# Kernel optimization log

Hardware: AMD Instinct MI355X
Metric: run time of the kernel (lower is better)

Reference implementation:

```python
import jax, jax.numpy as jnp
import numpy as np

B, S, H, D = 4, 1024, 16, 64
DIM = H * D          # 1024
FF_INNER = 4 * DIM   # 4096
ROT_BASE = 1000.0


def _l2norm(x):
    # F.normalize(p=2, dim=-1): x / max(||x||_2, 1e-12)
    n = jnp.linalg.norm(x, axis=-1, keepdims=True)
    return x / jnp.maximum(n, 1e-12)


def _rmsnorm(x):
    return x * jax.lax.rsqrt(jnp.mean(x * x, axis=-1, keepdims=True) + jnp.finfo(jnp.float32).eps)


def _rope_tables(seq, d, base):
    inv_freq = base ** (-(jnp.arange(0, d, 2, dtype=jnp.float32) / d))
    freqs = jnp.outer(jnp.arange(seq, dtype=jnp.float32), inv_freq)  # [S, D/2]
    # original caches cos/sin in bfloat16
    cos = jnp.cos(freqs).astype(jnp.bfloat16)[None, :, None, :]
    sin = jnp.sin(freqs).astype(jnp.bfloat16)[None, :, None, :]
    return cos, sin


def _rope(x, cos, sin):
    d = x.shape[3] // 2
    x1, x2 = x[..., :d], x[..., d:]
    y1 = x1 * cos + x2 * sin
    y2 = -x1 * sin + x2 * cos
    return jnp.concatenate([y1, y2], axis=3).astype(x.dtype)


def setup_inputs() -> dict:
    key = jax.random.key(0)
    ks = jax.random.split(key, 12)
    w = lambda k, shp: 0.02 * jax.random.normal(k, shp, dtype=jnp.float32)
    inp = {
        'h_states': jax.random.normal(ks[0], (B, S, DIM), dtype=jnp.float32),
        'attention_mask': jnp.tril(jnp.ones((S, S), dtype=jnp.float32))[None].repeat(B, axis=0),
        'Wq': w(ks[1], (DIM, DIM)), 'Wk': w(ks[2], (DIM, DIM)), 'Wv': w(ks[3], (DIM, DIM)),
        'WqB': w(ks[4], (DIM, DIM)), 'WkB': w(ks[5], (DIM, DIM)),
        'Wo': w(ks[6], (DIM, DIM)), 'bo': jnp.zeros((DIM,), jnp.float32),
        'Wff_in': w(ks[7], (DIM, 2 * FF_INNER)), 'bff_in': jnp.zeros((2 * FF_INNER,), jnp.float32),
        'Wff_out': w(ks[8], (FF_INNER, DIM)), 'bff_out': jnp.zeros((DIM,), jnp.float32),
        'learnedlambda': jnp.asarray(1.0, jnp.float32),
        'l2normscale': jnp.log(jnp.asarray(float(S) ** 2 - float(S), jnp.float32)),
    }
    return inp


def reference(h_states, attention_mask, Wq, Wk, Wv, WqB, WkB, Wo, bo,
              Wff_in, bff_in, Wff_out, bff_out, learnedlambda, l2normscale):
    inner = _rmsnorm(h_states)                               # layerwisenorm (rmsnorm, no affine)
    scale = D ** -0.5

    def proj(Wm):
        return (inner @ Wm).reshape(B, S, H, D)
    q, k, v = proj(Wq), proj(Wk), proj(Wv)
    bq, bk = proj(WqB), proj(WkB)

    cos, sin = _rope_tables(S, D, ROT_BASE)
    q = _rope(_l2norm(q), cos, sin)
    k = _rope(_l2norm(k), cos, sin)
    bq = _rope(_l2norm(bq), cos, sin)
    bk = _rope(_l2norm(bk), cos, sin)

    # main branch: causal softmax attention, scale=1, scaled by learned l2normscale
    scores = jnp.einsum('bihd,bjhd->bhij', q, k)             # [B,H,S,S]
    causal = jnp.tril(jnp.ones((S, S), dtype=bool))
    scores = jnp.where(causal, scores, -jnp.inf)
    attn = jax.nn.softmax(scores, axis=-1)
    y = l2normscale * jnp.einsum('bhij,bjhd->bihd', attn, v)  # [B,S,H,D]

    # bias branch: softmax-free masked scores @ ones == row-sum broadcast over D
    bscores = jnp.einsum('bihd,bjhd->bhij', bq, bk) * scale
    bscores = bscores * attention_mask[:, None, :, :]
    brow = bscores.sum(axis=-1)                               # [B,H,S]
    y = y + jnp.transpose(brow, (0, 2, 1))[..., None]         # broadcast over D

    attn_out = y.reshape(B, S, DIM) @ Wo + bo

    # SwiGLU FFN: chunk -> x, gate; silu(gate) * x
    u = inner @ Wff_in + bff_in
    xh, gate = jnp.split(u, 2, axis=-1)
    dense_out = (jax.nn.silu(gate) * xh) @ Wff_out + bff_out

    return h_states * learnedlambda + dense_out + attn_out
```

## Files before the change

### kernel.cpp

```cpp
#include <hip/hip_runtime.h>
#include <stdint.h>
#include <math.h>

typedef float f32x4 __attribute__((ext_vector_type(4)));
typedef short s16x8 __attribute__((ext_vector_type(8)));
typedef unsigned short bfu;

#define AS1q const __attribute__((address_space(1))) void*
#define AS3q __attribute__((address_space(3))) void*

static __device__ __forceinline__ float bf2f(bfu v) {
  return __uint_as_float(((unsigned int)v) << 16);
}
static __device__ __forceinline__ bfu f2bf(float f) {
  unsigned int u = __float_as_uint(f);
  return (bfu)((u + 0x7fffu + ((u >> 16) & 1u)) >> 16);
}

template <int MODE>
__global__ __launch_bounds__(256) void wconv_t(const float* __restrict__ W, bfu* __restrict__ Wt,
                                               int K, int N, int dstride, int dofs) {
  __shared__ float t[32][33];
  int tx = threadIdx.x & 31, ty = threadIdx.x >> 5;
  int nb = blockIdx.x * 32, kb = blockIdx.y * 32;
#pragma unroll
  for (int i = 0; i < 4; i++) {
    int r = ty + i * 8;
    t[r][tx] = W[(size_t)(kb + r) * N + nb + tx];
  }
  __syncthreads();
#pragma unroll
  for (int i = 0; i < 4; i++) {
    int r = ty + i * 8;
    int n = nb + r;
    int nd;
    if (MODE == 1) {
      int j = n & 4095, isg = n >> 12;
      nd = ((j >> 4) << 5) | (isg << 4) | (j & 15);
    } else nd = n;
    int k = kb + tx;
    int kp = (MODE == 2) ? (((k >> 5) << 5) | ((k & 15) << 1) | ((k >> 4) & 1)) : k;
    Wt[(size_t)nd * dstride + dofs + kp] = f2bf(t[tx][r]);
  }
}

struct Ptr5 { const float* p[5]; };
__global__ __launch_bounds__(256) void wconv5(Ptr5 srcs, bfu* __restrict__ dst) {
  __shared__ float t[32][33];
  const float* W = srcs.p[blockIdx.z];
  bfu* Wt = dst + ((size_t)blockIdx.z << 20);
  int tx = threadIdx.x & 31, ty = threadIdx.x >> 5;
  int nb = blockIdx.x * 32, kb = blockIdx.y * 32;
#pragma unroll
  for (int i = 0; i < 4; i++) {
    int r = ty + i * 8;
    t[r][tx] = W[(size_t)(kb + r) * 1024 + nb + tx];
  }
  __syncthreads();
#pragma unroll
  for (int i = 0; i < 4; i++) {
    int r = ty + i * 8;
    Wt[(size_t)(nb + r) * 1024 + kb + tx] = f2bf(t[tx][r]);
  }
}

__global__ void rope_tab(bfu* __restrict__ ct, bfu* __restrict__ st) {
  int idx = blockIdx.x * 256 + threadIdx.x;
  int s = idx >> 5, i = idx & 31;
  float f = powf(1000.0f, -(float)i / 32.0f);
  float fr = (float)s * f;
  ct[idx] = f2bf(cosf(fr));
  st[idx] = f2bf(sinf(fr));
}

__global__ __launch_bounds__(256) void rmsnorm_k(const float* __restrict__ h, bfu* __restrict__ inner) {
  int row = blockIdx.x;
  const float* hr = h + (size_t)row * 1024;
  f32x4 x = *reinterpret_cast<const f32x4*>(hr + threadIdx.x * 4);
  float ss = x[0] * x[0] + x[1] * x[1] + x[2] * x[2] + x[3] * x[3];
  for (int off = 32; off; off >>= 1) ss += __shfl_down(ss, off);
  __shared__ float wsum[4];
  int wave = threadIdx.x >> 6, lane = threadIdx.x & 63;
  if (lane == 0) wsum[wave] = ss;
  __syncthreads();
  float tot = wsum[0] + wsum[1] + wsum[2] + wsum[3];
  float r = rsqrtf(tot * (1.0f / 1024.0f) + 1.1920929e-07f);
  bfu* o = inner + (size_t)row * 1024 + threadIdx.x * 4;
  o[0] = f2bf(x[0] * r); o[1] = f2bf(x[1] * r);
  o[2] = f2bf(x[2] * r); o[3] = f2bf(x[3] * r);
}

template <int EPI>
__global__ __launch_bounds__(512, 2) void gemm256p(const bfu* __restrict__ A, const bfu* __restrict__ Bt,
                                                   bfu* __restrict__ outB,
                                                   const float* __restrict__ bias,
                                                   int M, int N, int K, int rbm, int rbn) {
  __shared__ __align__(16) char lds[131072];
  int nbx = N >> 8;
  int c = blockIdx.x & 7, rr = blockIdx.x >> 3;
  int ca = nbx / rbn;
  int bn0 = (c % ca) * rbn, bm0 = (c / ca) * rbm;
  int bm = bm0 + rr / rbn, bn = bn0 + rr % rbn;
  int tid = threadIdx.x, w = tid >> 6, lane = tid & 63;
  int wm = w >> 2, wn = w & 3;
  int g = lane >> 4, l15 = lane & 15;
  int NT = K >> 6;
  int NI = NT >> 1;

  f32x4 acc[8][4];
#pragma unroll
  for (int m = 0; m < 8; m++)
#pragma unroll
    for (int n = 0; n < 4; n++) acc[m][n] = (f32x4){0.f, 0.f, 0.f, 0.f};

  s16x8 af[4][2];
  s16x8 bfr[4][2];

  auto stage = [&](int mat, int kt, int hf) {
    if (kt >= NT) return;
    int d = kt & 1;
    const bfu* s0 = (mat == 0) ? A : Bt;
    int rowbase = ((mat == 0) ? bm : bn) * 256 + hf * 128;
    int k0 = kt << 6;
    char* base = lds + d * 65536 + mat * 32768 + hf * 16384;
#pragma unroll
    for (int r = 0; r < 2; r++) {
      int L = r * 512 + tid;
      int row = L >> 3, cc = L & 7;
      int kc = cc ^ (row & 7);
      const bfu* src = s0 + (size_t)(rowbase + row) * K + k0 + kc * 8;
      char* dst = base + r * 8192 + w * 1024;
      __builtin_amdgcn_global_load_lds((AS1q)src, (AS3q)dst, 16, 0, 0);
    }
  };

  auto ldA = [&](int d, int mh) {
    const char* base = lds + d * 65536 + wm * 16384;
#pragma unroll
    for (int mm = 0; mm < 4; mm++) {
      int row = mh * 64 + mm * 16 + l15;
#pragma unroll
      for (int ks = 0; ks < 2; ks++)
        af[mm][ks] = *reinterpret_cast<const s16x8*>(
            base + row * 128 + (((ks * 4 + g) ^ (row & 7)) << 4));
    }
  };
  auto ldB2 = [&](int d, int nh) {
    const char* base = lds + d * 65536 + 32768 + (wn >> 1) * 16384;
#pragma unroll
    for (int nn = 0; nn < 2; nn++) {
      int row = (wn & 1) * 64 + (nh * 2 + nn) * 16 + l15;
#pragma unroll
      for (int ks = 0; ks < 2; ks++)
        bfr[nh * 2 + nn][ks] = *reinterpret_cast<const s16x8*>(
            base + row * 128 + (((ks * 4 + g) ^ (row & 7)) << 4));
    }
  };
  auto mfma_q = [&](int mh, int nh) {
    asm volatile("s_waitcnt lgkmcnt(0)" ::: "memory");
    __builtin_amdgcn_sched_barrier(0);
    __builtin_amdgcn_s_barrier();
    __builtin_amdgcn_s_setprio(1);
#pragma unroll
    for (int mm = 0; mm < 4; mm++)
#pragma unroll
      for (int nn = 0; nn < 2; nn++) {
        int n = nh * 2 + nn, m = mh * 4 + mm;
#pragma unroll
        for (int ks = 0; ks < 2; ks++)
          acc[m][n] = __builtin_amdgcn_mfma_f32_16x16x32_bf16(af[mm][ks], bfr[n][ks], acc[m][n], 0, 0, 0);
      }
    __builtin_amdgcn_s_setprio(0);
    __builtin_amdgcn_sched_barrier(0);
  };

  stage(1, 0, 0); stage(0, 0, 0); stage(0, 0, 1); stage(1, 0, 1);
  stage(1, 1, 0); stage(1, 1, 1);
  asm volatile("s_waitcnt vmcnt(4)" ::: "memory");
  __builtin_amdgcn_s_barrier();
  __builtin_amdgcn_sched_barrier(0);

  for (int i = 0; i < NI; i++) {
    int t0 = 2 * i, t1 = 2 * i + 1;
    ldA(0, 0); ldB2(0, 0);
    stage(0, t1, 0);
    mfma_q(0, 0);
    ldB2(0, 1);
    stage(0, t1, 1);
    mfma_q(0, 1);
    ldA(0, 1);
    stage(1, t0 + 2, 0);
    mfma_q(1, 0);
    stage(1, t0 + 2, 1);
    mfma_q(1, 1);
    asm volatile("s_waitcnt vmcnt(4)" ::: "memory");
    __builtin_amdgcn_s_barrier();
    __builtin_amdgcn_sched_barrier(0);
    ldA(1, 0); ldB2(1, 0);
    stage(0, t0 + 2, 0);
    mfma_q(0, 0);
    ldB2(1, 1);
    stage(0, t0 + 2, 1);
    mfma_q(0, 1);
    ldA(1, 1);
    stage(1, t1 + 2, 0);
    mfma_q(1, 0);
    stage(1, t1 + 2, 1);
    mfma_q(1, 1);
    asm volatile("s_waitcnt vmcnt(4)" ::: "memory");
    __builtin_amdgcn_s_barrier();
    __builtin_amdgcn_sched_barrier(0);
  }

  int j0 = (bn * 8 + wn * 2) * 16 + l15;
  float bx0 = bias[j0], bg0 = bias[j0 + 4096];
  float bx1 = bias[j0 + 16], bg1 = bias[j0 + 16 + 4096];
  int cb = (bn * 4 + wn) * 32 + 2 * l15;
#pragma unroll
  for (int m = 0; m < 8; m++) {
#pragma unroll
    for (int r = 0; r < 4; r++) {
      int row = bm * 256 + wm * 128 + m * 16 + g * 4 + r;
      float xh0 = acc[m][0][r] + bx0, gt0 = acc[m][1][r] + bg0;
      float xh1 = acc[m][2][r] + bx1, gt1 = acc[m][3][r] + bg1;
      float s0 = gt0 / (1.0f + __expf(-gt0)) * xh0;
      float s1 = gt1 / (1.0f + __expf(-gt1)) * xh1;
      unsigned int pk = (unsigned int)f2bf(s0) | ((unsigned int)f2bf(s1) << 16);
      *reinterpret_cast<unsigned int*>(outB + (size_t)row * 5120 + cb) = pk;
    }
  }
}

__global__ __launch_bounds__(256, 3) void gemm128p(const bfu* __restrict__ A, const bfu* __restrict__ Bt,
                                                   bfu* __restrict__ qb, bfu* __restrict__ kb,
                                                   bfu* __restrict__ vb,
                                                   bfu* __restrict__ bqh, bfu* __restrict__ bkh,
                                                   const bfu* __restrict__ ct, const bfu* __restrict__ st,
                                                   int M, int N, int K, int rbm, int rbn) {
  __shared__ __align__(16) char lds[49152];
  int nbx = N >> 7;
  int c = blockIdx.x & 7, rr = blockIdx.x >> 3;
  int ca = nbx / rbn;
  int bn0 = (c % ca) * rbn, bm0 = (c / ca) * rbm;
  int bm = bm0 + rr / rbn, bn = bn0 + rr % rbn;
  int tid = threadIdx.x, w = tid >> 6, lane = tid & 63;
  int wm = w >> 1, wn = w & 1;
  int g = lane >> 4, l15 = lane & 15;
  int NT = K >> 5;

  f32x4 acc[4][4];
#pragma unroll
  for (int m = 0; m < 4; m++)
#pragma unroll
    for (int n = 0; n < 4; n++) acc[m][n] = (f32x4){0.f, 0.f, 0.f, 0.f};

  auto stage = [&](int buf, int t) {
    int k0 = t << 5;
#pragma unroll
    for (int r = 0; r < 2; r++) {
      int L = r * 256 + tid;
      int row = L >> 2, cc = L & 3;
      int kc = cc ^ (row & 3);
      const bfu* srcA = A + (size_t)(bm * 128 + row) * K + k0 + kc * 8;
      char* dstA = lds + buf * 16384 + r * 4096 + w * 1024;
      __builtin_amdgcn_global_load_lds((AS1q)srcA, (AS3q)dstA, 16, 0, 0);
      const bfu* srcB = Bt + (size_t)(bn * 128 + row) * K + k0 + kc * 8;
      char* dstB = lds + buf * 16384 + 8192 + r * 4096 + w * 1024;
      __builtin_amdgcn_global_load_lds((AS1q)srcB, (AS3q)dstB, 16, 0, 0);
    }
  };

  stage(0, 0); stage(1, 1);
  asm volatile("s_waitcnt vmcnt(4)" ::: "memory");
  __builtin_amdgcn_s_barrier();
  __builtin_amdgcn_sched_barrier(0);

  int bc = 0;
  for (int t = 0; t < NT; t++) {
    int bs = bc + 2; if (bs >= 3) bs -= 3;
    if (t + 2 < NT) stage(bs, t + 2);
    const char* la = lds + bc * 16384;
    const char* lb = la + 8192;
    s16x8 af[4], bfr[4];
#pragma unroll
    for (int m = 0; m < 4; m++) {
      int row = wm * 64 + m * 16 + l15;
      af[m] = *reinterpret_cast<const s16x8*>(la + row * 64 + ((g ^ (row & 3)) << 4));
    }
#pragma unroll
    for (int n = 0; n < 4; n++) {
      int row = wn * 64 + n * 16 + l15;
      bfr[n] = *reinterpret_cast<const s16x8*>(lb + row * 64 + ((g ^ (row & 3)) << 4));
    }
    asm volatile("s_waitcnt lgkmcnt(0)" ::: "memory");
    __builtin_amdgcn_sched_barrier(0);
    __builtin_amdgcn_s_setprio(1);
#pragma unroll
    for (int m = 0; m < 4; m++)
#pragma unroll
      for (int n = 0; n < 4; n++)
        acc[m][n] = __builtin_amdgcn_mfma_f32_16x16x32_bf16(af[m], bfr[n], acc[m][n], 0, 0, 0);
    __builtin_amdgcn_s_setprio(0);
    __builtin_amdgcn_sched_barrier(0);
    if (t < NT - 2) { asm volatile("s_waitcnt vmcnt(4)" ::: "memory"); }
    else            { asm volatile("s_waitcnt vmcnt(0)" ::: "memory"); }
    __builtin_amdgcn_s_barrier();
    __builtin_amdgcn_sched_barrier(0);
    bc++; if (bc == 3) bc = 0;
  }

  int which = bn >> 3;
  int hh = (bn & 7) * 2 + wn;
#pragma unroll
  for (int m = 0; m < 4; m++) {
#pragma unroll
    for (int r = 0; r < 4; r++) {
      int row = bm * 128 + wm * 64 + m * 16 + g * 4 + r;
      int s = row & 1023, b = row >> 10;
      float a0 = acc[m][0][r], a1 = acc[m][1][r];
      float a2 = acc[m][2][r], a3 = acc[m][3][r];
      if (which == 2) {
        unsigned long long pk =
            (unsigned long long)((unsigned int)f2bf(a0) | ((unsigned int)f2bf(a1) << 16)) |
            ((unsigned long long)((unsigned int)f2bf(a2) | ((unsigned int)f2bf(a3) << 16)) << 32);
        *reinterpret_cast<unsigned long long*>(
            vb + ((size_t)(b * 1024 + s) << 10) + (hh << 6) + (l15 << 2)) = pk;
      } else {
        float ss = a0 * a0 + a1 * a1 + a2 * a2 + a3 * a3;
        ss += __shfl_xor(ss, 1); ss += __shfl_xor(ss, 2);
        ss += __shfl_xor(ss, 4); ss += __shfl_xor(ss, 8);
        float inv = 1.0f / fmaxf(sqrtf(ss), 1e-12f);
        float xn0 = a0 * inv, xn1 = a1 * inv, xn2 = a2 * inv, xn3 = a3 * inv;
        float c0 = bf2f(ct[(s << 5) + l15]),      s0v = bf2f(st[(s << 5) + l15]);
        float c1 = bf2f(ct[(s << 5) + 16 + l15]), s1v = bf2f(st[(s << 5) + 16 + l15]);
        float o0 = xn0 * c0 + xn2 * s0v;
        float o1 = xn1 * c1 + xn3 * s1v;
        float o2 = xn2 * c0 - xn0 * s0v;
        float o3 = xn3 * c1 - xn1 * s1v;
        unsigned long long pk =
            (unsigned long long)((unsigned int)f2bf(o0) | ((unsigned int)f2bf(o1) << 16)) |
            ((unsigned long long)((unsigned int)f2bf(o2) | ((unsigned int)f2bf(o3) << 16)) << 32);
        size_t base = ((((size_t)((b << 4) + hh) << 10) + s) << 6) + (l15 << 2);
        bfu* dst = (which == 0) ? qb : (which == 1) ? kb : (which == 3) ? bqh : bkh;
        *reinterpret_cast<unsigned long long*>(dst + base) = pk;
      }
    }
  }
}

__global__ __launch_bounds__(256, 3) void gemm128f(const bfu* __restrict__ A, const bfu* __restrict__ Bt,
                                                   float* __restrict__ out,
                                                   const float* __restrict__ b1,
                                                   const float* __restrict__ b2,
                                                   const float* __restrict__ lam,
                                                   const float* __restrict__ h,
                                                   int M, int N, int K, int rbm, int rbn) {
  __shared__ __align__(16) char lds[49152];
  int nbx = N >> 7;
  int c = blockIdx.x & 7, rr = blockIdx.x >> 3;
  int ca = nbx / rbn;
  int bn0 = (c % ca) * rbn, bm0 = (c / ca) * rbm;
  int bm = bm0 + rr / rbn, bn = bn0 + rr % rbn;
  int tid = threadIdx.x, w = tid >> 6, lane = tid & 63;
  int wm = w >> 1, wn = w & 1;
  int g = lane >> 4, l15 = lane & 15;
  int NT = K >> 5;

  f32x4 acc[4][4];
#pragma unroll
  for (int m = 0; m < 4; m++)
#pragma unroll
    for (int n = 0; n < 4; n++) acc[m][n] = (f32x4){0.f, 0.f, 0.f, 0.f};

  auto stage = [&](int buf, int t) {
    int k0 = t << 5;
#pragma unroll
    for (int r = 0; r < 2; r++) {
      int L = r * 256 + tid;
      int row = L >> 2, cc = L & 3;
      int kc = cc ^ (row & 3);
      const bfu* srcA = A + (size_t)(bm * 128 + row) * K + k0 + kc * 8;
      char* dstA = lds + buf * 16384 + r * 4096 + w * 1024;
      __builtin_amdgcn_global_load_lds((AS1q)srcA, (AS3q)dstA, 16, 0, 0);
      const bfu* srcB = Bt + (size_t)(bn * 128 + row) * K + k0 + kc * 8;
      char* dstB = lds + buf * 16384 + 8192 + r * 4096 + w * 1024;
      __builtin_amdgcn_global_load_lds((AS1q)srcB, (AS3q)dstB, 16, 0, 0);
    }
  };

  stage(0, 0); stage(1, 1);
  asm volatile("s_waitcnt vmcnt(4)" ::: "memory");
  __builtin_amdgcn_s_barrier();
  __builtin_amdgcn_sched_barrier(0);

  int bc = 0;
  for (int t = 0; t < NT; t++) {
    int bs = bc + 2; if (bs >= 3) bs -= 3;
    if (t + 2 < NT) stage(bs, t + 2);
    const char* la = lds + bc * 16384;
    const char* lb = la + 8192;
    s16x8 af[4], bfr[4];
#pragma unroll
    for (int m = 0; m < 4; m++) {
      int row = wm * 64 + m * 16 + l15;
      af[m] = *reinterpret_cast<const s16x8*>(la + row * 64 + ((g ^ (row & 3)) << 4));
    }
#pragma unroll
    for (int n = 0; n < 4; n++) {
      int row = wn * 64 + n * 16 + l15;
      bfr[n] = *reinterpret_cast<const s16x8*>(lb + row * 64 + ((g ^ (row & 3)) << 4));
    }
    asm volatile("s_waitcnt lgkmcnt(0)" ::: "memory");
    __builtin_amdgcn_sched_barrier(0);
    __builtin_amdgcn_s_setprio(1);
#pragma unroll
    for (int m = 0; m < 4; m++)
#pragma unroll
      for (int n = 0; n < 4; n++)
        acc[m][n] = __builtin_amdgcn_mfma_f32_16x16x32_bf16(af[m], bfr[n], acc[m][n], 0, 0, 0);
    __builtin_amdgcn_s_setprio(0);
    __builtin_amdgcn_sched_barrier(0);
    if (t < NT - 2) { asm volatile("s_waitcnt vmcnt(4)" ::: "memory"); }
    else            { asm volatile("s_waitcnt vmcnt(0)" ::: "memory"); }
    __builtin_amdgcn_s_barrier();
    __builtin_amdgcn_sched_barrier(0);
    bc++; if (bc == 3) bc = 0;
  }

  float lv = lam[0];
#pragma unroll
  for (int m = 0; m < 4; m++) {
    int row = bm * 128 + wm * 64 + m * 16 + g * 4;
#pragma unroll
    for (int n = 0; n < 4; n++) {
      int col = bn * 128 + wn * 64 + n * 16 + l15;
      float bb = b1[col] + b2[col];
#pragma unroll
      for (int r = 0; r < 4; r++) {
        size_t o = (size_t)(row + r) * 1024 + col;
        out[o] = acc[m][n][r] + bb + lv * h[o];
      }
    }
  }
}

__global__ __launch_bounds__(256) void vtrans(const bfu* __restrict__ vb, bfu* __restrict__ vT) {
  __shared__ bfu t[64][66];
  int bh = blockIdx.y, stile = blockIdx.x;
  int b = bh >> 4, h = bh & 15;
  int s0 = stile << 6;
  for (int ii = threadIdx.x; ii < 4096; ii += 256) {
    int r = ii >> 6, d = ii & 63;
    t[r][d] = vb[(size_t)(b * 1024 + s0 + r) * 1024 + (h << 6) + d];
  }
  __syncthreads();
  for (int ii = threadIdx.x; ii < 4096; ii += 256) {
    int d = ii >> 6, sc = ii & 63;
    int psrc = ((d & 15) << 2) | (d >> 4);
    vT[((size_t)(bh * 64 + d) << 10) + s0 + sc] = t[sc][psrc];
  }
}

__global__ void bk_chunksum(const bfu* __restrict__ bk, float* __restrict__ csum) {
  int cid = blockIdx.x;
  int bh = cid >> 3, c = cid & 7, lane = threadIdx.x;
  float s = 0.f;
  const bfu* p = bk + ((size_t)bh * 1024 + c * 128) * 64 + lane;
  for (int j = 0; j < 128; j++) s += bf2f(p[(size_t)j * 64]);
  csum[cid * 64 + lane] = s;
}

__global__ void brow_k(const bfu* __restrict__ bq, const bfu* __restrict__ bk,
                       const float* __restrict__ csum, float* __restrict__ brow) {
  int cid = blockIdx.x;
  int bh = cid >> 3, c = cid & 7, lane = threadIdx.x;
  float p = 0.f;
  for (int cc = 0; cc < c; cc++) p += csum[(bh * 8 + cc) * 64 + lane];
  size_t base = ((size_t)bh * 1024 + c * 128) * 64 + lane;
  for (int j = 0; j < 128; j++) {
    p += bf2f(bk[base + (size_t)j * 64]);
    float t = bf2f(bq[base + (size_t)j * 64]) * p;
#pragma unroll
    for (int m2 = 1; m2 < 64; m2 <<= 1) t += __shfl_xor(t, m2);
    if (lane == 0) brow[bh * 1024 + c * 128 + j] = 0.125f * t;
  }
}

__global__ __launch_bounds__(256) void flash_k(const bfu* __restrict__ q, const bfu* __restrict__ k,
                                               const bfu* __restrict__ vT,
                                               const float* __restrict__ brow,
                                               const float* __restrict__ l2p,
                                               bfu* __restrict__ y) {
  __shared__ __align__(16) bfu P[4][2][16][72];
  int id = blockIdx.x;
  int sub = id & 255;
  int qt = (id >> 8) ? 7 - (sub >> 6) : (sub >> 6);
  int bh = sub & 63;
  int wave = threadIdx.x >> 6, lane = threadIdx.x & 63;
  int g = lane >> 4, l15 = lane & 15;
  const size_t bhofs = (size_t)bh << 16;
  int rt0 = qt * 128 + wave * 32;

  s16x8 aq[2][2];
#pragma unroll
  for (int m = 0; m < 2; m++)
#pragma unroll
    for (int ks = 0; ks < 2; ks++)
      aq[m][ks] = *reinterpret_cast<const s16x8*>(
          q + bhofs + (size_t)(rt0 + m * 16 + l15) * 64 + ks * 32 + g * 8);

  f32x4 O[2][4];
  float mr[2][4], lr[2][4];
#pragma unroll
  for (int m = 0; m < 2; m++)
#pragma unroll
    for (int r = 0; r < 4; r++) { O[m][r] = (f32x4){0.f, 0.f, 0.f, 0.f}; mr[m][r] = -3.0e38f; lr[m][r] = 0.f; }

  s16x8 kA[4][2], kB[4][2];
  auto loadK = [&](s16x8 (&kd)[4][2], int jt) {
#pragma unroll
    for (int nt = 0; nt < 4; nt++)
#pragma unroll
      for (int ks = 0; ks < 2; ks++)
        kd[nt][ks] = *reinterpret_cast<const s16x8*>(
            k + bhofs + (size_t)(jt * 64 + nt * 16 + l15) * 64 + ks * 32 + g * 8);
  };

  int njt = 2 * qt + 2;
  loadK(kA, 0);

  auto body = [&](int jt, s16x8 (&kc)[4][2], s16x8 (&kn)[4][2], bool pf) {
    s16x8 vv[4][2];
#pragma unroll
    for (int nt = 0; nt < 4; nt++)
#pragma unroll
      for (int ks = 0; ks < 2; ks++)
        vv[nt][ks] = *reinterpret_cast<const s16x8*>(
            vT + ((size_t)(bh * 64 + nt * 16 + l15) << 10) + jt * 64 + ks * 32 + g * 8);

    bool act[2] = { jt * 64 <= rt0 + 15, jt * 64 <= rt0 + 31 };
    f32x4 sfr[2][4];
#pragma unroll
    for (int m = 0; m < 2; m++) {
      if (!act[m]) continue;
#pragma unroll
      for (int nt = 0; nt < 4; nt++) {
        sfr[m][nt] = (f32x4){0.f, 0.f, 0.f, 0.f};
#pragma unroll
        for (int ks = 0; ks < 2; ks++)
          sfr[m][nt] = __builtin_amdgcn_mfma_f32_16x16x32_bf16(aq[m][ks], kc[nt][ks], sfr[m][nt], 0, 0, 0);
      }
    }
    if (pf) loadK(kn, jt + 1);

#pragma unroll
    for (int m = 0; m < 2; m++) {
      if (!act[m]) continue;
      int rtm = rt0 + m * 16;
      if (jt * 64 + 63 > rtm) {
#pragma unroll
        for (int ntn = 0; ntn < 4; ntn++)
#pragma unroll
          for (int r = 0; r < 4; r++)
            if (jt * 64 + ntn * 16 + l15 > rtm + g * 4 + r) sfr[m][ntn][r] = -1e30f;
      }
      float alpha[4];
#pragma unroll
      for (int r = 0; r < 4; r++) {
        float v = fmaxf(fmaxf(sfr[m][0][r], sfr[m][1][r]), fmaxf(sfr[m][2][r], sfr[m][3][r]));
#pragma unroll
        for (int m2 = 1; m2 < 16; m2 <<= 1) v = fmaxf(v, __shfl_xor(v, m2));
        float mn = fmaxf(mr[m][r], v);
        alpha[r] = __expf(mr[m][r] - mn);
        mr[m][r] = mn;
      }
#pragma unroll
      for (int r = 0; r < 4; r++) {
        float rs = 0.f;
#pragma unroll
        for (int ntn = 0; ntn < 4; ntn++) {
          float e = __expf(sfr[m][ntn][r] - mr[m][r]);
          rs += e;
          P[wave][m][g * 4 + r][ntn * 16 + l15] = f2bf(e);
        }
#pragma unroll
        for (int m2 = 1; m2 < 16; m2 <<= 1) rs += __shfl_xor(rs, m2);
        lr[m][r] = lr[m][r] * alpha[r] + rs;
#pragma unroll
        for (int ntn = 0; ntn < 4; ntn++) O[m][ntn][r] *= alpha[r];
      }
    }
    asm volatile("s_waitcnt lgkmcnt(0)" ::: "memory");
    __builtin_amdgcn_sched_barrier(0);
#pragma unroll
    for (int m = 0; m < 2; m++) {
      if (!act[m]) continue;
      s16x8 pa[2];
#pragma unroll
      for (int ks = 0; ks < 2; ks++)
        pa[ks] = *reinterpret_cast<const s16x8*>(&P[wave][m][l15][ks * 32 + g * 8]);
#pragma unroll
      for (int nt = 0; nt < 4; nt++)
#pragma unroll
        for (int ks = 0; ks < 2; ks++)
          O[m][nt] = __builtin_amdgcn_mfma_f32_16x16x32_bf16(pa[ks], vv[nt][ks], O[m][nt], 0, 0, 0);
    }
  };

  for (int jt = 0; jt < njt; jt += 2) {
    body(jt, kA, kB, true);
    body(jt + 1, kB, kA, jt + 2 < njt);
  }

  float l2ns = l2p[0];
  int b = bh >> 4, hq = bh & 15;
#pragma unroll
  for (int m = 0; m < 2; m++)
#pragma unroll
    for (int r = 0; r < 4; r++) {
      int rowg = rt0 + m * 16 + g * 4 + r;
      float br = brow[bh * 1024 + rowg];
      float sc = l2ns / lr[m][r];
      float v0 = O[m][0][r] * sc + br;
      float v1 = O[m][1][r] * sc + br;
      float v2 = O[m][2][r] * sc + br;
      float v3 = O[m][3][r] * sc + br;
      unsigned int p01 = (unsigned int)f2bf(v0) | ((unsigned int)f2bf(v1) << 16);
      unsigned int p23 = (unsigned int)f2bf(v2) | ((unsigned int)f2bf(v3) << 16);
      size_t base = (size_t)(b * 1024 + rowg) * 5120 + 4096 + hq * 64;
      *reinterpret_cast<unsigned int*>(y + base + 2 * l15) = p01;
      *reinterpret_cast<unsigned int*>(y + base + 32 + 2 * l15) = p23;
    }
}

extern "C" void kernel_launch(void* const* d_in, const int* in_sizes, int n_in,
                              void* d_out, int out_size, void* d_ws, size_t ws_size,
                              hipStream_t stream) {
  const float* h      = (const float*)d_in[0];
  const float* Wq     = (const float*)d_in[2];
  const float* Wk     = (const float*)d_in[3];
  const float* Wv     = (const float*)d_in[4];
  const float* WqB    = (const float*)d_in[5];
  const float* WkB    = (const float*)d_in[6];
  const float* Wo     = (const float*)d_in[7];
  const float* bo     = (const float*)d_in[8];
  const float* Wffin  = (const float*)d_in[9];
  const float* bffin  = (const float*)d_in[10];
  const float* Wffout = (const float*)d_in[11];
  const float* bffout = (const float*)d_in[12];
  const float* lam    = (const float*)d_in[13];
  const float* l2ns   = (const float*)d_in[14];
  float* out = (float*)d_out;

  char* ws = (char*)d_ws;
  size_t off = 0;
  auto alloc = [&](size_t bytes) { void* p = ws + off; off += bytes; return p; };
  bfu* wt5   = (bfu*)alloc(5ull * 1024 * 1024 * 2);
  bfu* wtfi  = (bfu*)alloc(8192ull * 1024 * 2);
  bfu* wtfoc = (bfu*)alloc(1024ull * 5120 * 2);
  bfu* cosb  = (bfu*)alloc(1024ull * 32 * 2);
  bfu* sinb  = (bfu*)alloc(1024ull * 32 * 2);
  bfu* inner = (bfu*)alloc(4096ull * 1024 * 2);
  bfu* qb    = (bfu*)alloc(64ull * 1024 * 64 * 2);
  bfu* kb    = (bfu*)alloc(64ull * 1024 * 64 * 2);
  bfu* vb    = (bfu*)alloc(4096ull * 1024 * 2);
  bfu* vtb   = (bfu*)alloc(64ull * 1024 * 64 * 2);
  bfu* bqh   = (bfu*)alloc(64ull * 1024 * 64 * 2);
  bfu* bkh   = (bfu*)alloc(64ull * 1024 * 64 * 2);
  float* csum  = (float*)alloc(64ull * 8 * 64 * 4);
  float* browb = (float*)alloc(64ull * 1024 * 4);
  bfu* AB    = (bfu*)alloc(4096ull * 5120 * 2);

  Ptr5 p5; p5.p[0] = Wq; p5.p[1] = Wk; p5.p[2] = Wv; p5.p[3] = WqB; p5.p[4] = WkB;
  wconv5<<<dim3(32, 32, 5), 256, 0, stream>>>(p5, wt5);
  wconv_t<1><<<dim3(256, 32), 256, 0, stream>>>(Wffin, wtfi, 1024, 8192, 1024, 0);
  wconv_t<2><<<dim3(32, 128), 256, 0, stream>>>(Wffout, wtfoc, 4096, 1024, 5120, 0);
  wconv_t<2><<<dim3(32, 32), 256, 0, stream>>>(Wo, wtfoc, 1024, 1024, 5120, 4096);
  rope_tab<<<128, 256, 0, stream>>>(cosb, sinb);
  rmsnorm_k<<<4096, 256, 0, stream>>>(h, inner);

  gemm128p<<<dim3(1280), 256, 0, stream>>>(inner, wt5, qb, kb, vb, bqh, bkh, cosb, sinb,
                                           4096, 5120, 1024, 32, 5);

  vtrans<<<dim3(16, 64), 256, 0, stream>>>(vb, vtb);
  bk_chunksum<<<512, 64, 0, stream>>>(bkh, csum);
  brow_k<<<512, 64, 0, stream>>>(bqh, bkh, csum, browb);

  flash_k<<<dim3(512), 256, 0, stream>>>(qb, kb, vtb, browb, l2ns, AB);

  gemm256p<1><<<dim3(512), 512, 0, stream>>>(inner, wtfi, AB, bffin,
                                             4096, 8192, 1024, 8, 8);

  gemm128f<<<dim3(256), 256, 0, stream>>>(AB, wtfoc, out, bffout, bo, lam, h,
                                          4096, 1024, 5120, 8, 4);
}
```

Measured before the change: 360.2 us.

## Split-K the final output GEMM into three partials with a separate reduce kernel

The final GEMM (M=4096, N=1024, K=5120) previously ran only 256 tiles, fewer than the GPU's compute units, so it underfilled the device. It now splits K into three chunks (54/53/53 k-tiles) across 768 blocks, each writing fp32 partials. A new reduce kernel sums the partials and applies the bias and the lambda*h residual. This trades better occupancy for about 48MB of extra partial-buffer traffic and one more kernel launch.

```diff
diff --git a/kernel.cpp b/kernel.cpp
--- a/kernel.cpp
+++ b/kernel.cpp
@@ -348,23 +348,20 @@
   }
 }
 
-__global__ __launch_bounds__(256, 3) void gemm128f(const bfu* __restrict__ A, const bfu* __restrict__ Bt,
-                                                   float* __restrict__ out,
-                                                   const float* __restrict__ b1,
-                                                   const float* __restrict__ b2,
-                                                   const float* __restrict__ lam,
-                                                   const float* __restrict__ h,
-                                                   int M, int N, int K, int rbm, int rbn) {
+__global__ __launch_bounds__(256, 3) void gemm128s(const bfu* __restrict__ A, const bfu* __restrict__ Bt,
+                                                   float* __restrict__ part,
+                                                   int M, int N, int K) {
   __shared__ __align__(16) char lds[49152];
-  int nbx = N >> 7;
-  int c = blockIdx.x & 7, rr = blockIdx.x >> 3;
-  int ca = nbx / rbn;
-  int bn0 = (c % ca) * rbn, bm0 = (c / ca) * rbm;
-  int bm = bm0 + rr / rbn, bn = bn0 + rr % rbn;
+  int ks = blockIdx.x >> 8;
+  int sub = blockIdx.x & 255;
+  int c = sub & 7, rr = sub >> 3;
+  int bn0 = (c & 1) * 4, bm0 = (c >> 1) * 8;
+  int bm = bm0 + (rr >> 2), bn = bn0 + (rr & 3);
   int tid = threadIdx.x, w = tid >> 6, lane = tid & 63;
   int wm = w >> 1, wn = w & 1;
   int g = lane >> 4, l15 = lane & 15;
-  int NT = K >> 5;
+  int kt0 = (ks == 0) ? 0 : (54 + 53 * (ks - 1));
+  int kt1 = (ks == 0) ? 54 : (kt0 + 53);
 
   f32x4 acc[4][4];
 #pragma unroll
@@ -388,15 +385,15 @@
     }
   };
 
-  stage(0, 0); stage(1, 1);
+  stage(0, kt0); stage(1, kt0 + 1);
   asm volatile("s_waitcnt vmcnt(4)" ::: "memory");
   __builtin_amdgcn_s_barrier();
   __builtin_amdgcn_sched_barrier(0);
 
   int bc = 0;
-  for (int t = 0; t < NT; t++) {
+  for (int t = kt0; t < kt1; t++) {
     int bs = bc + 2; if (bs >= 3) bs -= 3;
-    if (t + 2 < NT) stage(bs, t + 2);
+    if (t + 2 < kt1) stage(bs, t + 2);
     const char* la = lds + bc * 16384;
     const char* lb = la + 8192;
     s16x8 af[4], bfr[4];
@@ -420,28 +417,45 @@
         acc[m][n] = __builtin_amdgcn_mfma_f32_16x16x32_bf16(af[m], bfr[n], acc[m][n], 0, 0, 0);
     __builtin_amdgcn_s_setprio(0);
     __builtin_amdgcn_sched_barrier(0);
-    if (t < NT - 2) { asm volatile("s_waitcnt vmcnt(4)" ::: "memory"); }
-    else            { asm volatile("s_waitcnt vmcnt(0)" ::: "memory"); }
+    if (t < kt1 - 2) { asm volatile("s_waitcnt vmcnt(4)" ::: "memory"); }
+    else             { asm volatile("s_waitcnt vmcnt(0)" ::: "memory"); }
     __builtin_amdgcn_s_barrier();
     __builtin_amdgcn_sched_barrier(0);
     bc++; if (bc == 3) bc = 0;
   }
 
-  float lv = lam[0];
+  float* dst = part + (size_t)ks * M * N;
 #pragma unroll
   for (int m = 0; m < 4; m++) {
     int row = bm * 128 + wm * 64 + m * 16 + g * 4;
 #pragma unroll
     for (int n = 0; n < 4; n++) {
       int col = bn * 128 + wn * 64 + n * 16 + l15;
-      float bb = b1[col] + b2[col];
-#pragma unroll
-      for (int r = 0; r < 4; r++) {
-        size_t o = (size_t)(row + r) * 1024 + col;
-        out[o] = acc[m][n][r] + bb + lv * h[o];
-      }
-    }
-  }
+#pragma unroll
+      for (int r = 0; r < 4; r++)
+        dst[(size_t)(row + r) * N + col] = acc[m][n][r];
+    }
+  }
+}
+
+__global__ __launch_bounds__(256) void reduce_out(const float* __restrict__ part,
+                                                  const float* __restrict__ b1,
+                                                  const float* __restrict__ b2,
+                                                  const float* __restrict__ lam,
+                                                  const float* __restrict__ h,
+                                                  float* __restrict__ out) {
+  float lv = lam[0];
+  int i = blockIdx.x * 256 + threadIdx.x;
+  f32x4 p0 = *reinterpret_cast<const f32x4*>(part + (size_t)i * 4);
+  f32x4 p1 = *reinterpret_cast<const f32x4*>(part + 4194304ull + (size_t)i * 4);
+  f32x4 p2 = *reinterpret_cast<const f32x4*>(part + 8388608ull + (size_t)i * 4);
+  f32x4 hv = *reinterpret_cast<const f32x4*>(h + (size_t)i * 4);
+  int col = (i * 4) & 1023;
+  f32x4 o;
+#pragma unroll
+  for (int j = 0; j < 4; j++)
+    o[j] = p0[j] + p1[j] + p2[j] + b1[col + j] + b2[col + j] + lv * hv[j];
+  *reinterpret_cast<f32x4*>(out + (size_t)i * 4) = o;
 }
 
 __global__ __launch_bounds__(256) void vtrans(const bfu* __restrict__ vb, bfu* __restrict__ vT) {
@@ -670,6 +684,7 @@
   float* csum  = (float*)alloc(64ull * 8 * 64 * 4);
   float* browb = (float*)alloc(64ull * 1024 * 4);
   bfu* AB    = (bfu*)alloc(4096ull * 5120 * 2);
+  float* part = (float*)alloc(3ull * 4096 * 1024 * 4);
 
   Ptr5 p5; p5.p[0] = Wq; p5.p[1] = Wk; p5.p[2] = Wv; p5.p[3] = WqB; p5.p[4] = WkB;
   wconv5<<<dim3(32, 32, 5), 256, 0, stream>>>(p5, wt5);
@@ -691,6 +706,6 @@
   gemm256p<1><<<dim3(512), 512, 0, stream>>>(inner, wtfi, AB, bffin,
                                              4096, 8192, 1024, 8, 8);
 
-  gemm128f<<<dim3(256), 256, 0, stream>>>(AB, wtfoc, out, bffout, bo, lam, h,
-                                          4096, 1024, 5120, 8, 4);
-}
+  gemm128s<<<dim3(768), 256, 0, stream>>>(AB, wtfoc, part, 4096, 1024, 5120);
+  reduce_out<<<dim3(4096), 256, 0, stream>>>(part, bffout, bo, lam, h, out);
+}
```

After: 367.8 us. 2.1% more time.

## Merge prologue kernels into one launch and fuse bias row-sum kernels

Applied to the files above, without the earlier changes.

Six prologue kernels (weight conversions, RoPE table, rmsnorm) become a single launch that dispatches on block index. The two-pass bias row-sum (chunk sums, then prefix scan) becomes one kernel with one block per (batch, head) that shares chunk sums through LDS. This cuts launch count and the global scratch round-trip. The GEMM's last iteration now waits for all outstanding loads instead of leaving four in flight. The row-sum kernel now runs only 64 blocks, so it has less parallelism.

```diff
diff --git a/kernel.cpp b/kernel.cpp
--- a/kernel.cpp
+++ b/kernel.cpp
@@ -17,77 +17,78 @@
   return (bfu)((u + 0x7fffu + ((u >> 16) & 1u)) >> 16);
 }
 
-template <int MODE>
-__global__ __launch_bounds__(256) void wconv_t(const float* __restrict__ W, bfu* __restrict__ Wt,
-                                               int K, int N, int dstride, int dofs) {
-  __shared__ float t[32][33];
-  int tx = threadIdx.x & 31, ty = threadIdx.x >> 5;
-  int nb = blockIdx.x * 32, kb = blockIdx.y * 32;
-#pragma unroll
-  for (int i = 0; i < 4; i++) {
-    int r = ty + i * 8;
-    t[r][tx] = W[(size_t)(kb + r) * N + nb + tx];
-  }
-  __syncthreads();
-#pragma unroll
-  for (int i = 0; i < 4; i++) {
-    int r = ty + i * 8;
-    int n = nb + r;
-    int nd;
-    if (MODE == 1) {
-      int j = n & 4095, isg = n >> 12;
-      nd = ((j >> 4) << 5) | (isg << 4) | (j & 15);
-    } else nd = n;
-    int k = kb + tx;
-    int kp = (MODE == 2) ? (((k >> 5) << 5) | ((k & 15) << 1) | ((k >> 4) & 1)) : k;
-    Wt[(size_t)nd * dstride + dofs + kp] = f2bf(t[tx][r]);
-  }
-}
-
-struct Ptr5 { const float* p[5]; };
-__global__ __launch_bounds__(256) void wconv5(Ptr5 srcs, bfu* __restrict__ dst) {
-  __shared__ float t[32][33];
-  const float* W = srcs.p[blockIdx.z];
-  bfu* Wt = dst + ((size_t)blockIdx.z << 20);
-  int tx = threadIdx.x & 31, ty = threadIdx.x >> 5;
-  int nb = blockIdx.x * 32, kb = blockIdx.y * 32;
-#pragma unroll
-  for (int i = 0; i < 4; i++) {
-    int r = ty + i * 8;
-    t[r][tx] = W[(size_t)(kb + r) * 1024 + nb + tx];
-  }
-  __syncthreads();
-#pragma unroll
-  for (int i = 0; i < 4; i++) {
-    int r = ty + i * 8;
-    Wt[(size_t)(nb + r) * 1024 + kb + tx] = f2bf(t[tx][r]);
-  }
-}
-
-__global__ void rope_tab(bfu* __restrict__ ct, bfu* __restrict__ st) {
-  int idx = blockIdx.x * 256 + threadIdx.x;
-  int s = idx >> 5, i = idx & 31;
-  float f = powf(1000.0f, -(float)i / 32.0f);
-  float fr = (float)s * f;
-  ct[idx] = f2bf(cosf(fr));
-  st[idx] = f2bf(sinf(fr));
-}
-
-__global__ __launch_bounds__(256) void rmsnorm_k(const float* __restrict__ h, bfu* __restrict__ inner) {
-  int row = blockIdx.x;
-  const float* hr = h + (size_t)row * 1024;
-  f32x4 x = *reinterpret_cast<const f32x4*>(hr + threadIdx.x * 4);
-  float ss = x[0] * x[0] + x[1] * x[1] + x[2] * x[2] + x[3] * x[3];
-  for (int off = 32; off; off >>= 1) ss += __shfl_down(ss, off);
-  __shared__ float wsum[4];
-  int wave = threadIdx.x >> 6, lane = threadIdx.x & 63;
-  if (lane == 0) wsum[wave] = ss;
-  __syncthreads();
-  float tot = wsum[0] + wsum[1] + wsum[2] + wsum[3];
-  float r = rsqrtf(tot * (1.0f / 1024.0f) + 1.1920929e-07f);
-  bfu* o = inner + (size_t)row * 1024 + threadIdx.x * 4;
-  o[0] = f2bf(x[0] * r); o[1] = f2bf(x[1] * r);
-  o[2] = f2bf(x[2] * r); o[3] = f2bf(x[3] * r);
+struct PreArgs {
+  const float* w5[5];
+  const float* Wffin;
+  const float* Wffout;
+  const float* Wo;
+  const float* h;
+  bfu* wt5; bfu* wtfi; bfu* wtfoc;
+  bfu* cosb; bfu* sinb; bfu* inner;
+};
+__global__ __launch_bounds__(256) void prologue_k(PreArgs a) {
+  __shared__ float shmem[32 * 33];
+  int id = blockIdx.x;
+  if (id < 18432) {
+    const float* W; bfu* Wt; int K, N, dstride, dofs, mode, nb, kb;
+    if (id < 5120) {
+      int z = id >> 10, rem = id & 1023;
+      W = a.w5[z]; Wt = a.wt5 + ((size_t)z << 20);
+      K = 1024; N = 1024; dstride = 1024; dofs = 0; mode = 0;
+      nb = (rem & 31) << 5; kb = (rem >> 5) << 5;
+    } else if (id < 13312) {
+      int id2 = id - 5120;
+      W = a.Wffin; Wt = a.wtfi; K = 1024; N = 8192; dstride = 1024; dofs = 0; mode = 1;
+      nb = (id2 & 255) << 5; kb = (id2 >> 8) << 5;
+    } else if (id < 17408) {
+      int id3 = id - 13312;
+      W = a.Wffout; Wt = a.wtfoc; K = 4096; N = 1024; dstride = 5120; dofs = 0; mode = 2;
+      nb = (id3 & 31) << 5; kb = (id3 >> 5) << 5;
+    } else {
+      int id4 = id - 17408;
+      W = a.Wo; Wt = a.wtfoc; K = 1024; N = 1024; dstride = 5120; dofs = 4096; mode = 2;
+      nb = (id4 & 31) << 5; kb = (id4 >> 5) << 5;
+    }
+    float (*t)[33] = reinterpret_cast<float(*)[33]>(shmem);
+    int tx = threadIdx.x & 31, ty = threadIdx.x >> 5;
+#pragma unroll
+    for (int i = 0; i < 4; i++) {
+      int r = ty + i * 8;
+      t[r][tx] = W[(size_t)(kb + r) * N + nb + tx];
+    }
+    __syncthreads();
+#pragma unroll
+    for (int i = 0; i < 4; i++) {
+      int r = ty + i * 8;
+      int n = nb + r;
+      int nd = n;
+      if (mode == 1) { int j = n & 4095, isg = n >> 12; nd = ((j >> 4) << 5) | (isg << 4) | (j & 15); }
+      int k = kb + tx;
+      int kp = (mode == 2) ? (((k >> 5) << 5) | ((k & 15) << 1) | ((k >> 4) & 1)) : k;
+      Wt[(size_t)nd * dstride + dofs + kp] = f2bf(t[tx][r]);
+    }
+  } else if (id < 18560) {
+    int idx = (id - 18432) * 256 + threadIdx.x;
+    int s = idx >> 5, i = idx & 31;
+    float f = powf(1000.0f, -(float)i / 32.0f);
+    float fr = (float)s * f;
+    a.cosb[idx] = f2bf(cosf(fr));
+    a.sinb[idx] = f2bf(sinf(fr));
+  } else {
+    int row = id - 18560;
+    const float* hr = a.h + (size_t)row * 1024;
+    f32x4 x = *reinterpret_cast<const f32x4*>(hr + threadIdx.x * 4);
+    float ss = x[0] * x[0] + x[1] * x[1] + x[2] * x[2] + x[3] * x[3];
+    for (int off = 32; off; off >>= 1) ss += __shfl_down(ss, off);
+    int wave = threadIdx.x >> 6, lane = threadIdx.x & 63;
+    if (lane == 0) shmem[wave] = ss;
+    __syncthreads();
+    float tot = shmem[0] + shmem[1] + shmem[2] + shmem[3];
+    float r = rsqrtf(tot * (1.0f / 1024.0f) + 1.1920929e-07f);
+    bfu* o = a.inner + (size_t)row * 1024 + threadIdx.x * 4;
+    o[0] = f2bf(x[0] * r); o[1] = f2bf(x[1] * r);
+    o[2] = f2bf(x[2] * r); o[3] = f2bf(x[3] * r);
+  }
 }
 
 template <int EPI>
@@ -182,6 +183,7 @@
 
   for (int i = 0; i < NI; i++) {
     int t0 = 2 * i, t1 = 2 * i + 1;
+    bool last = (i == NI - 1);
     ldA(0, 0); ldB2(0, 0);
     stage(0, t1, 0);
     mfma_q(0, 0);
@@ -193,7 +195,8 @@
     mfma_q(1, 0);
     stage(1, t0 + 2, 1);
     mfma_q(1, 1);
-    asm volatile("s_waitcnt vmcnt(4)" ::: "memory");
+    if (last) { asm volatile("s_waitcnt vmcnt(0)" ::: "memory"); }
+    else      { asm volatile("s_waitcnt vmcnt(4)" ::: "memory"); }
     __builtin_amdgcn_s_barrier();
     __builtin_amdgcn_sched_barrier(0);
     ldA(1, 0); ldB2(1, 0);
@@ -461,28 +464,24 @@
   }
 }
 
-__global__ void bk_chunksum(const bfu* __restrict__ bk, float* __restrict__ csum) {
-  int cid = blockIdx.x;
-  int bh = cid >> 3, c = cid & 7, lane = threadIdx.x;
+__global__ __launch_bounds__(512) void brow_all(const bfu* __restrict__ bq, const bfu* __restrict__ bk,
+                                                float* __restrict__ brow) {
+  __shared__ float csums[8][64];
+  int bh = blockIdx.x;
+  int wave = threadIdx.x >> 6, lane = threadIdx.x & 63;
+  size_t base = ((size_t)bh * 1024 + wave * 128) * 64 + lane;
   float s = 0.f;
-  const bfu* p = bk + ((size_t)bh * 1024 + c * 128) * 64 + lane;
-  for (int j = 0; j < 128; j++) s += bf2f(p[(size_t)j * 64]);
-  csum[cid * 64 + lane] = s;
-}
-
-__global__ void brow_k(const bfu* __restrict__ bq, const bfu* __restrict__ bk,
-                       const float* __restrict__ csum, float* __restrict__ brow) {
-  int cid = blockIdx.x;
-  int bh = cid >> 3, c = cid & 7, lane = threadIdx.x;
+  for (int j = 0; j < 128; j++) s += bf2f(bk[base + (size_t)j * 64]);
+  csums[wave][lane] = s;
+  __syncthreads();
   float p = 0.f;
-  for (int cc = 0; cc < c; cc++) p += csum[(bh * 8 + cc) * 64 + lane];
-  size_t base = ((size_t)bh * 1024 + c * 128) * 64 + lane;
+  for (int cc = 0; cc < wave; cc++) p += csums[cc][lane];
   for (int j = 0; j < 128; j++) {
     p += bf2f(bk[base + (size_t)j * 64]);
     float t = bf2f(bq[base + (size_t)j * 64]) * p;
 #pragma unroll
     for (int m2 = 1; m2 < 64; m2 <<= 1) t += __shfl_xor(t, m2);
-    if (lane == 0) brow[bh * 1024 + c * 128 + j] = 0.125f * t;
+    if (lane == 0) brow[bh * 1024 + wave * 128 + j] = 0.125f * t;
   }
 }
 
@@ -667,24 +666,21 @@
   bfu* vtb   = (bfu*)alloc(64ull * 1024 * 64 * 2);
   bfu* bqh   = (bfu*)alloc(64ull * 1024 * 64 * 2);
   bfu* bkh   = (bfu*)alloc(64ull * 1024 * 64 * 2);
-  float* csum  = (float*)alloc(64ull * 8 * 64 * 4);
   float* browb = (float*)alloc(64ull * 1024 * 4);
   bfu* AB    = (bfu*)alloc(4096ull * 5120 * 2);
 
-  Ptr5 p5; p5.p[0] = Wq; p5.p[1] = Wk; p5.p[2] = Wv; p5.p[3] = WqB; p5.p[4] = WkB;
-  wconv5<<<dim3(32, 32, 5), 256, 0, stream>>>(p5, wt5);
-  wconv_t<1><<<dim3(256, 32), 256, 0, stream>>>(Wffin, wtfi, 1024, 8192, 1024, 0);
-  wconv_t<2><<<dim3(32, 128), 256, 0, stream>>>(Wffout, wtfoc, 4096, 1024, 5120, 0);
-  wconv_t<2><<<dim3(32, 32), 256, 0, stream>>>(Wo, wtfoc, 1024, 1024, 5120, 4096);
-  rope_tab<<<128, 256, 0, stream>>>(cosb, sinb);
-  rmsnorm_k<<<4096, 256, 0, stream>>>(h, inner);
+  PreArgs pa;
+  pa.w5[0] = Wq; pa.w5[1] = Wk; pa.w5[2] = Wv; pa.w5[3] = WqB; pa.w5[4] = WkB;
+  pa.Wffin = Wffin; pa.Wffout = Wffout; pa.Wo = Wo; pa.h = h;
+  pa.wt5 = wt5; pa.wtfi = wtfi; pa.wtfoc = wtfoc;
+  pa.cosb = cosb; pa.sinb = sinb; pa.inner = inner;
+  prologue_k<<<dim3(22656), 256, 0, stream>>>(pa);
 
   gemm128p<<<dim3(1280), 256, 0, stream>>>(inner, wt5, qb, kb, vb, bqh, bkh, cosb, sinb,
                                            4096, 5120, 1024, 32, 5);
 
   vtrans<<<dim3(16, 64), 256, 0, stream>>>(vb, vtb);
-  bk_chunksum<<<512, 64, 0, stream>>>(bkh, csum);
-  brow_k<<<512, 64, 0, stream>>>(bqh, bkh, csum, browb);
+  brow_all<<<dim3(64), 512, 0, stream>>>(bqh, bkh, browb);
 
   flash_k<<<dim3(512), 256, 0, stream>>>(qb, kb, vtb, browb, l2ns, AB);
 
```

Measured after the change: 348.8 us. 3.2% less time.
